# Kernel optimization log

Measured on AMD Instinct MI355X. Metric: run time of the kernel, lower is better.

Reference implementation:

```python
import jax, jax.numpy as jnp
import numpy as np

V, D, H, HS, BLK, L = 50257, 768, 12, 64, 1024, 6
B, S = 4, 1024
EPS = 1e-5


def layer_norm(x, g, b):
    mu = jnp.mean(x, axis=-1, keepdims=True)
    var = jnp.mean(jnp.square(x - mu), axis=-1, keepdims=True)
    return (x - mu) * jax.lax.rsqrt(var + EPS) * g + b


def setup_inputs() -> dict:
    key = jax.random.key(0)
    ks = jax.random.split(key, 24)
    s = 0.02
    inp = {
        "idx": jax.random.randint(ks[0], (B, S), 0, V),
        "tok_emb": jax.random.normal(ks[1], (V, D), jnp.float32) * s,
        "pos_emb": jax.random.normal(ks[2], (BLK, D), jnp.float32) * s,
        "Wq": jax.random.normal(ks[3], (L, H, D, HS), jnp.float32) * s,
        "bq": jnp.zeros((L, H, HS), jnp.float32),
        "Wk": jax.random.normal(ks[4], (L, H, D, HS), jnp.float32) * s,
        "bk": jnp.zeros((L, H, HS), jnp.float32),
        "Wv": jax.random.normal(ks[5], (L, H, D, HS), jnp.float32) * s,
        "bv": jnp.zeros((L, H, HS), jnp.float32),
        "Wproj": jax.random.normal(ks[6], (L, D, D), jnp.float32) * s,
        "bproj": jnp.zeros((L, D), jnp.float32),
        "ln1_g": jnp.ones((L, D), jnp.float32),
        "ln1_b": jnp.zeros((L, D), jnp.float32),
        "ln2_g": jnp.ones((L, D), jnp.float32),
        "ln2_b": jnp.zeros((L, D), jnp.float32),
        "Wf1": jax.random.normal(ks[7], (L, D, 4 * D), jnp.float32) * s,
        "bf1": jnp.zeros((L, 4 * D), jnp.float32),
        "Wf2": jax.random.normal(ks[8], (L, 4 * D, D), jnp.float32) * s,
        "bf2": jnp.zeros((L, D), jnp.float32),
        "lnf_g": jnp.ones((D,), jnp.float32),
        "lnf_b": jnp.zeros((D,), jnp.float32),
        "Wlm": jax.random.normal(ks[9], (V, D), jnp.float32) * s,
    }
    return inp


def attention(x, Wq, bq, Wk, bk, Wv, bv, Wproj, bproj):
    # x: [B,S,D]; per-head projections stacked over H
    q = jnp.einsum("bsd,hdk->bhsk", x, Wq) + bq[:, None, :]
    k = jnp.einsum("bsd,hdk->bhsk", x, Wk) + bk[:, None, :]
    v = jnp.einsum("bsd,hdk->bhsk", x, Wv) + bv[:, None, :]
    scores = jnp.einsum("bhsk,bhtk->bhst", q, k)  # [B,H,S,S]
    s = x.shape[1]
    mask = jnp.tril(jnp.ones((s, s), bool))
    # original: masked_fill(-inf) THEN divide by sqrt(head_size) -- equivalent
    scores = jnp.where(mask, scores, -jnp.inf) / np.sqrt(HS)
    w = jax.nn.softmax(scores, axis=-1)
    out = jnp.einsum("bhst,bhtk->bhsk", w, v)
    out = out.transpose(0, 2, 1, 3).reshape(x.shape[0], s, H * HS)
    return out @ Wproj + bproj


def reference(idx, tok_emb, pos_emb, Wq, bq, Wk, bk, Wv, bv, Wproj, bproj,
              ln1_g, ln1_b, ln2_g, ln2_b, Wf1, bf1, Wf2, bf2, lnf_g, lnf_b, Wlm):
    s = idx.shape[1]
    x = tok_emb[idx] + pos_emb[:s]
    for i in range(L):
        h = layer_norm(x, ln1_g[i], ln1_b[i])
        x = x + attention(h, Wq[i], bq[i], Wk[i], bk[i], Wv[i], bv[i], Wproj[i], bproj[i])
        h = layer_norm(x, ln2_g[i], ln2_b[i])
        x = x + (jax.nn.gelu(h @ Wf1[i] + bf1[i], approximate=False) @ Wf2[i] + bf2[i])
    x = layer_norm(x, lnf_g, lnf_b)
    logits = x @ Wlm.T  # [B,S,V]
    return logits
```

## Files before the change

### kernel.cpp

```cpp
#include <hip/hip_runtime.h>
#include <hip/hip_bf16.h>
#include <math.h>

#define D_MODEL 768
#define N_HEAD  12
#define HEAD    64
#define SEQ     1024
#define NLAYER  6
#define BATCH   4
#define NROWS   (BATCH*SEQ)
#define VOCAB   50257
#define VPAD    50432
#define DFFN    3072
#define DQKV    2304

typedef __attribute__((ext_vector_type(8))) __bf16 bf16x8;
typedef __attribute__((ext_vector_type(4))) float f32x4;
typedef __attribute__((ext_vector_type(4))) unsigned short u16x4;
typedef __attribute__((ext_vector_type(8))) unsigned short u16x8;

__device__ inline unsigned short f2bf(float x) {
    __hip_bfloat16 h = __float2bfloat16(x);
    return *reinterpret_cast<unsigned short*>(&h);
}

__global__ __launch_bounds__(256)
void embed_kernel(const int* __restrict__ idx, const float* __restrict__ tok,
                  const float* __restrict__ pos, float* __restrict__ x) {
    int row = blockIdx.x;
    int t = idx[row];
    int s = row & (SEQ - 1);
    const float* tp = tok + (size_t)t * D_MODEL;
    const float* pp = pos + (size_t)s * D_MODEL;
    float* xp = x + (size_t)row * D_MODEL;
    for (int i = threadIdx.x; i < D_MODEL; i += 256) xp[i] = tp[i] + pp[i];
}

__global__ __launch_bounds__(256)
void ln_kernel(const float* __restrict__ in, const float* __restrict__ gw,
               const float* __restrict__ bw, unsigned short* __restrict__ out) {
    int row = blockIdx.x;
    int tid = threadIdx.x;
    const float* x = in + (size_t)row * D_MODEL;
    float v0 = x[tid], v1 = x[tid + 256], v2 = x[tid + 512];
    float s  = v0 + v1 + v2;
    float sq = v0*v0 + v1*v1 + v2*v2;
    #pragma unroll
    for (int o = 1; o < 64; o <<= 1) { s += __shfl_xor(s, o); sq += __shfl_xor(sq, o); }
    __shared__ float red[8];
    int wave = tid >> 6;
    if ((tid & 63) == 0) { red[wave] = s; red[4 + wave] = sq; }
    __syncthreads();
    s  = red[0] + red[1] + red[2] + red[3];
    sq = red[4] + red[5] + red[6] + red[7];
    float mean = s * (1.0f / D_MODEL);
    float var  = sq * (1.0f / D_MODEL) - mean * mean;
    float rstd = rsqrtf(var + 1e-5f);
    unsigned short* op = out + (size_t)row * D_MODEL;
    op[tid]       = f2bf((v0 - mean) * rstd * gw[tid]       + bw[tid]);
    op[tid + 256] = f2bf((v1 - mean) * rstd * gw[tid + 256] + bw[tid + 256]);
    op[tid + 512] = f2bf((v2 - mean) * rstd * gw[tid + 512] + bw[tid + 512]);
}

template<int MODE>
__global__ __launch_bounds__(256)
void conv_transpose(const float* __restrict__ in, unsigned short* __restrict__ out,
                    int K, int N, size_t inLstride, size_t outLstride) {
    __shared__ float t[64][65];
    const int tid = threadIdx.x;
    const int n0 = blockIdx.x * 64, k0 = blockIdx.y * 64;
    const float* ip = in + blockIdx.z * inLstride;
    unsigned short* op = out + blockIdx.z * outLstride;
    {
        const int kk = tid >> 4, nq = tid & 15;
        #pragma unroll
        for (int p = 0; p < 4; ++p) {
            int k = kk + p * 16;
            float4 v;
            if (MODE == 0) v = *reinterpret_cast<const float4*>(&ip[(size_t)(k0 + k) * N + n0 + nq * 4]);
            else           v = *reinterpret_cast<const float4*>(&ip[((size_t)(n0 >> 6) * K + (k0 + k)) * 64 + nq * 4]);
            t[k][nq * 4 + 0] = v.x; t[k][nq * 4 + 1] = v.y;
            t[k][nq * 4 + 2] = v.z; t[k][nq * 4 + 3] = v.w;
        }
    }
    __syncthreads();
    {
        const int n = tid >> 2, kq = tid & 3;
        unsigned short buf[16];
        #pragma unroll
        for (int j = 0; j < 16; ++j) buf[j] = f2bf(t[kq * 16 + j][n]);
        unsigned short* dst = &op[(size_t)(n0 + n) * K + k0 + kq * 16];
        *reinterpret_cast<u16x8*>(dst)     = *reinterpret_cast<u16x8*>(&buf[0]);
        *reinterpret_cast<u16x8*>(dst + 8) = *reinterpret_cast<u16x8*>(&buf[8]);
    }
}

__global__ __launch_bounds__(256)
void conv_lm(const float* __restrict__ in, unsigned short* __restrict__ out) {
    const int nchunks = VPAD * D_MODEL / 4;
    const int vchunks = VOCAB * D_MODEL / 4;
    for (int i = blockIdx.x * 256 + threadIdx.x; i < nchunks; i += gridDim.x * 256) {
        u16x4 o;
        if (i < vchunks) {
            float4 v = reinterpret_cast<const float4*>(in)[i];
            o[0] = f2bf(v.x); o[1] = f2bf(v.y); o[2] = f2bf(v.z); o[3] = f2bf(v.w);
        } else { o[0] = 0; o[1] = 0; o[2] = 0; o[3] = 0; }
        reinterpret_cast<u16x4*>(out)[i] = o;
    }
}

__global__ __launch_bounds__(256)
void conv_bias(const float* __restrict__ bq, const float* __restrict__ bk,
               const float* __restrict__ bv, float* __restrict__ out) {
    int i = blockIdx.x * 256 + threadIdx.x;
    if (i >= NLAYER * DQKV) return;
    int l = i / DQKV, n = i % DQKV;
    float v;
    if (n < 768)        v = bq[l * 768 + n];
    else if (n < 1536)  v = bk[l * 768 + n - 768];
    else                v = bv[l * 768 + n - 1536];
    out[i] = v;
}

__global__ __launch_bounds__(512)
void gemm256_mfma(const unsigned short* __restrict__ A, const unsigned short* __restrict__ B,
                  float* __restrict__ C, int M, int N, int K) {
    __shared__ unsigned short smem[2 * 2 * 16384];
    const int nwg = gridDim.x;
    const int t0 = (blockIdx.x & 7) * (nwg >> 3) + (blockIdx.x >> 3);
    const int MT = M >> 8;
    const int NBX = nwg / MT;
    const int srsize = NBX * 8;
    const int sr = t0 / srsize;
    const int rem = t0 - sr * srsize;
    const int bx = rem >> 3;
    const int by = sr * 8 + (rem & 7);
    const int bm = by * 256, bn = bx * 256;
    const int tid = threadIdx.x;
    const int l = tid & 63, w = tid >> 6;
    const int wm = w >> 2, wn = w & 3;
    const int lr = l & 15, lc = l >> 4;
    f32x4 acc[8][4] = {};

    auto stage = [&](int k0, int buf) {
        #pragma unroll
        for (int p = 0; p < 4; ++p) {
            int d16 = p * 512 + tid;
            int row = d16 >> 3, cph = d16 & 7;
            int clog = cph ^ (row & 7);
            const unsigned short* ga = A + (size_t)(bm + row) * K + k0 + clog * 8;
            __builtin_amdgcn_global_load_lds(
                (const __attribute__((address_space(1))) unsigned int*)ga,
                (__attribute__((address_space(3))) unsigned int*)(&smem[buf * 32768 + d16 * 8]), 16, 0, 0);
        }
        #pragma unroll
        for (int p = 0; p < 4; ++p) {
            int d16 = p * 512 + tid;
            int row = d16 >> 3, cph = d16 & 7;
            int clog = cph ^ (row & 7);
            const unsigned short* gb = B + (size_t)(bn + row) * K + k0 + clog * 8;
            __builtin_amdgcn_global_load_lds(
                (const __attribute__((address_space(1))) unsigned int*)gb,
                (__attribute__((address_space(3))) unsigned int*)(&smem[buf * 32768 + 16384 + d16 * 8]), 16, 0, 0);
        }
    };

    auto compute = [&](int buf) {
        const unsigned short* Ab = &smem[buf * 32768];
        const unsigned short* Bb = &smem[buf * 32768 + 16384];
        bf16x8 bfr[2][4];
        #pragma unroll
        for (int ks = 0; ks < 2; ++ks)
            #pragma unroll
            for (int j = 0; j < 4; ++j) {
                int col = wn * 64 + j * 16 + lr;
                bfr[ks][j] = *reinterpret_cast<const bf16x8*>(
                    &Bb[col * 64 + (((ks * 4 + lc) ^ (col & 7)) * 8)]);
            }
        #pragma unroll
        for (int qm = 0; qm < 2; ++qm) {
            bf16x8 af[2][4];
            #pragma unroll
            for (int ks = 0; ks < 2; ++ks)
                #pragma unroll
                for (int mi = 0; mi < 4; ++mi) {
                    int row = wm * 128 + qm * 64 + mi * 16 + lr;
                    af[ks][mi] = *reinterpret_cast<const bf16x8*>(
                        &Ab[row * 64 + (((ks * 4 + lc) ^ (row & 7)) * 8)]);
                }
            __builtin_amdgcn_s_setprio(1);
            #pragma unroll
            for (int ks = 0; ks < 2; ++ks)
                #pragma unroll
                for (int mi = 0; mi < 4; ++mi)
                    #pragma unroll
                    for (int j = 0; j < 4; ++j)
                        acc[qm * 4 + mi][j] = __builtin_amdgcn_mfma_f32_16x16x32_bf16(
                            bfr[ks][j], af[ks][mi], acc[qm * 4 + mi][j], 0, 0, 0);
            __builtin_amdgcn_s_setprio(0);
        }
    };

    const int NT = K >> 6;
    stage(0, 0);
    asm volatile("s_waitcnt vmcnt(0)" ::: "memory");
    __builtin_amdgcn_s_barrier();
    for (int t = 0; t < NT; ++t) {
        const int cur = t & 1;
        if (t + 1 < NT) stage((t + 1) << 6, cur ^ 1);
        compute(cur);
        if (t + 1 < NT) {
            asm volatile("s_waitcnt vmcnt(0)" ::: "memory");
            __builtin_amdgcn_s_barrier();
        }
    }

    #pragma unroll
    for (int i = 0; i < 8; ++i) {
        const int row = bm + wm * 128 + i * 16 + lr;
        #pragma unroll
        for (int j = 0; j < 4; ++j) {
            const int colb = bn + wn * 64 + j * 16 + lc * 4;
            if (colb + 3 < N) {
                *reinterpret_cast<f32x4*>(&C[(size_t)row * N + colb]) = acc[i][j];
            } else {
                #pragma unroll
                for (int r = 0; r < 4; ++r)
                    if (colb + r < N) C[(size_t)row * N + colb + r] = acc[i][j][r];
            }
        }
    }
}

template<int BN, int OUTF , bool GELU, bool RES>
__global__ __launch_bounds__(256)
void gemm_sched(const unsigned short* __restrict__ A, const unsigned short* __restrict__ B,
                const float* __restrict__ bias, const float* __restrict__ res,
                void* __restrict__ Cout, int M, int N, int K) {
    constexpr int ABUF = 64 * 64;
    constexpr int TBUF = (64 + BN) * 64;
    constexpr int NI = BN / 32;
    __shared__ unsigned short smem[2 * TBUF];
    const int nwg = gridDim.x;
    const int t0 = (blockIdx.x & 7) * (nwg >> 3) + (blockIdx.x >> 3);
    const int MT = M >> 6;
    const int NBX = nwg / MT;
    const int srsize = NBX * 8;
    const int sr = t0 / srsize;
    const int rem = t0 - sr * srsize;
    const int bx = rem >> 3;
    const int by = sr * 8 + (rem & 7);
    const int bm = by * 64, bn = bx * BN;
    const int tid = threadIdx.x;
    const int l = tid & 63, w = tid >> 6;
    const int wr = (w & 1) * 32;
    const int wc = (w >> 1) * (BN / 2);
    const int lr = l & 15, lc = l >> 4;
    f32x4 acc[2][NI] = {};

    auto stage = [&](int k0, int buf) {
        #pragma unroll
        for (int p = 0; p < 2; ++p) {
            int d16 = p * 256 + tid;
            int row = d16 >> 3, cph = d16 & 7;
            int clog = cph ^ (row & 7);
            const unsigned short* ga = A + (size_t)(bm + row) * K + k0 + clog * 8;
            __builtin_amdgcn_global_load_lds(
                (const __attribute__((address_space(1))) unsigned int*)ga,
                (__attribute__((address_space(3))) unsigned int*)(&smem[buf * TBUF + d16 * 8]), 16, 0, 0);
        }
        #pragma unroll
        for (int p = 0; p < BN / 32; ++p) {
            int d16 = p * 256 + tid;
            int row = d16 >> 3, cph = d16 & 7;
            int clog = cph ^ (row & 7);
            const unsigned short* gb = B + (size_t)(bn + row) * K + k0 + clog * 8;
            __builtin_amdgcn_global_load_lds(
                (const __attribute__((address_space(1))) unsigned int*)gb,
                (__attribute__((address_space(3))) unsigned int*)(&smem[buf * TBUF + ABUF + d16 * 8]), 16, 0, 0);
        }
    };

    auto compute = [&](int buf) {
        const unsigned short* Ab = &smem[buf * TBUF];
        const unsigned short* Bb = &smem[buf * TBUF + ABUF];
        #pragma unroll
        for (int ks = 0; ks < 2; ++ks) {
            bf16x8 af[2], bfr[NI];
            #pragma unroll
            for (int mi = 0; mi < 2; ++mi) {
                int row = wr + mi * 16 + lr;
                af[mi] = *reinterpret_cast<const bf16x8*>(
                    &Ab[row * 64 + (((ks * 4 + lc) ^ (row & 7)) * 8)]);
            }
            #pragma unroll
            for (int ni = 0; ni < NI; ++ni) {
                int col = wc + ni * 16 + lr;
                bfr[ni] = *reinterpret_cast<const bf16x8*>(
                    &Bb[col * 64 + (((ks * 4 + lc) ^ (col & 7)) * 8)]);
            }
            __builtin_amdgcn_s_setprio(1);
            #pragma unroll
            for (int mi = 0; mi < 2; ++mi)
                #pragma unroll
                for (int ni = 0; ni < NI; ++ni)
                    acc[mi][ni] = __builtin_amdgcn_mfma_f32_16x16x32_bf16(
                        bfr[ni], af[mi], acc[mi][ni], 0, 0, 0);
            __builtin_amdgcn_s_setprio(0);
        }
    };

    const int NT = K >> 6;
    stage(0, 0);
    asm volatile("s_waitcnt vmcnt(0)" ::: "memory");
    __builtin_amdgcn_s_barrier();
    for (int t = 0; t < NT; ++t) {
        const int cur = t & 1;
        if (t + 1 < NT) stage((t + 1) << 6, cur ^ 1);
        compute(cur);
        if (t + 1 < NT) {
            asm volatile("s_waitcnt vmcnt(0)" ::: "memory");
            __builtin_amdgcn_s_barrier();
        }
    }

    #pragma unroll
    for (int mi = 0; mi < 2; ++mi) {
        const int row = bm + wr + mi * 16 + lr;
        #pragma unroll
        for (int ni = 0; ni < NI; ++ni) {
            const int colb = bn + wc + ni * 16 + lc * 4;
            f32x4 v = acc[mi][ni];
            if (bias) v += *reinterpret_cast<const f32x4*>(&bias[colb]);
            if (GELU) {
                #pragma unroll
                for (int r = 0; r < 4; ++r)
                    v[r] = 0.5f * v[r] * (1.0f + erff(v[r] * 0.70710678118654752f));
            }
            if (RES) v += *reinterpret_cast<const f32x4*>(&res[(size_t)row * N + colb]);
            if (OUTF == 0) {
                *reinterpret_cast<f32x4*>(&((float*)Cout)[(size_t)row * N + colb]) = v;
            } else {
                u16x4 o;
                o[0] = f2bf(v[0]); o[1] = f2bf(v[1]); o[2] = f2bf(v[2]); o[3] = f2bf(v[3]);
                *reinterpret_cast<u16x4*>(&((unsigned short*)Cout)[(size_t)row * N + colb]) = o;
            }
        }
    }
}

__global__ __launch_bounds__(512)
void attn_mfma(const unsigned short* __restrict__ qkv, unsigned short* __restrict__ ao) {
    const int qt = gridDim.x - 1 - blockIdx.x;
    const int h = blockIdx.y, b = blockIdx.z;
    const int tid = threadIdx.x;
    const int w = tid >> 6, l = tid & 63;
    const int c = l & 15, g = l >> 4;

    __shared__ unsigned short Ks[2][32 * 64];
    __shared__ unsigned short Vt[2][64 * 40];
    __shared__ unsigned int   Ps[8][16 * 20];

    const unsigned short* base = qkv + (size_t)(b * SEQ) * DQKV + h * HEAD;
    const int q0 = qt * 128 + w * 16;

    bf16x8 qf[2];
    {
        const unsigned short* qp = base + (size_t)(q0 + c) * DQKV + g * 8;
        qf[0] = *reinterpret_cast<const bf16x8*>(qp);
        qf[1] = *reinterpret_cast<const bf16x8*>(qp + 32);
    }

    f32x4 o_acc[4] = {};
    float m_run[4]  = {-INFINITY, -INFINITY, -INFINITY, -INFINITY};
    float l_run[4]  = {0.f, 0.f, 0.f, 0.f};

    const int srow = tid >> 4, sch8 = tid & 15;
    const int scj = sch8 >> 1, sh = sch8 & 1;
    const int vd = tid & 63, vw = tid >> 6;

    u16x4 kreg;
    unsigned short vreg[4];
    auto loadKV = [&](int kt) {
        kreg = *reinterpret_cast<const u16x4*>(
            base + (size_t)(kt * 32 + srow) * DQKV + 768 + sch8 * 4);
        #pragma unroll
        for (int j = 0; j < 4; ++j)
            vreg[j] = base[(size_t)(kt * 32 + vw * 4 + j) * DQKV + 1536 + vd];
    };

    const int nkt = 4 * qt + 4;
    loadKV(0);
    for (int kt = 0; kt < nkt; ++kt) {
        const int bf = kt & 1;
        *reinterpret_cast<u16x4*>(&Ks[bf][srow * 64 + ((scj ^ (srow & 7)) * 8) + sh * 4]) = kreg;
        {
            uint2 pk;
            pk.x = vreg[0] | ((unsigned)vreg[1] << 16);
            pk.y = vreg[2] | ((unsigned)vreg[3] << 16);
            *reinterpret_cast<uint2*>(&Vt[bf][vd * 40 + vw * 4]) = pk;
        }
        __syncthreads();
        if (kt + 1 < nkt) loadKV(kt + 1);

        f32x4 s_acc[2] = {};
        #pragma unroll
        for (int t = 0; t < 2; ++t) {
            const int kr = t * 16 + c;
            #pragma unroll
            for (int ks = 0; ks < 2; ++ks) {
                bf16x8 kf = *reinterpret_cast<const bf16x8*>(
                    &Ks[bf][kr * 64 + (((ks * 4 + g) ^ (kr & 7)) * 8)]);
                s_acc[t] = __builtin_amdgcn_mfma_f32_16x16x32_bf16(qf[ks], kf, s_acc[t], 0, 0, 0);
            }
        }
        float sc[2][4];
        #pragma unroll
        for (int t = 0; t < 2; ++t) {
            const int kglob = kt * 32 + t * 16 + c;
            #pragma unroll
            for (int r = 0; r < 4; ++r) {
                float v = s_acc[t][r] * 0.125f;
                sc[t][r] = (kglob > q0 + g * 4 + r) ? -1e30f : v;
            }
        }
        float pout[2][4];
        #pragma unroll
        for (int r = 0; r < 4; ++r) {
            float tmax = fmaxf(sc[0][r], sc[1][r]);
            #pragma unroll
            for (int ms = 1; ms < 16; ms <<= 1) tmax = fmaxf(tmax, __shfl_xor(tmax, ms));
            float mnew = fmaxf(m_run[r], tmax);
            float alpha = __expf(m_run[r] - mnew);
            float p0 = __expf(sc[0][r] - mnew);
            float p1 = __expf(sc[1][r] - mnew);
            float psum = p0 + p1;
            #pragma unroll
            for (int ms = 1; ms < 16; ms <<= 1) psum += __shfl_xor(psum, ms);
            l_run[r] = l_run[r] * alpha + psum;
            m_run[r] = mnew;
            #pragma unroll
            for (int dt = 0; dt < 4; ++dt) o_acc[dt][r] *= alpha;
            pout[0][r] = p0; pout[1][r] = p1;
        }
        #pragma unroll
        for (int t = 0; t < 2; ++t) {
            #pragma unroll
            for (int r = 0; r < 4; ++r) {
                int my = f2bf(pout[t][r]);
                int part = __shfl_xor(my, 1);
                unsigned int word = (c & 1) ? ((unsigned)(part & 0xffff) | ((unsigned)my << 16))
                                            : ((unsigned)(my & 0xffff) | ((unsigned)part << 16));
                Ps[w][(g * 4 + r) * 20 + t * 8 + (c >> 1)] = word;
            }
        }
        uint4 praw = *reinterpret_cast<const uint4*>(&Ps[w][c * 20 + g * 4]);
        bf16x8 pf = *reinterpret_cast<const bf16x8*>(&praw);
        #pragma unroll
        for (int dt = 0; dt < 4; ++dt) {
            bf16x8 vf = *reinterpret_cast<const bf16x8*>(&Vt[bf][(dt * 16 + c) * 40 + g * 8]);
            o_acc[dt] = __builtin_amdgcn_mfma_f32_16x16x32_bf16(pf, vf, o_acc[dt], 0, 0, 0);
        }
    }

    float inv[4];
    #pragma unroll
    for (int r = 0; r < 4; ++r) inv[r] = 1.0f / l_run[r];
    #pragma unroll
    for (int r = 0; r < 4; ++r) {
        unsigned short* op = ao + (size_t)(b * SEQ + q0 + g * 4 + r) * D_MODEL + h * HEAD + c;
        #pragma unroll
        for (int dt = 0; dt < 4; ++dt)
            op[dt * 16] = f2bf(o_acc[dt][r] * inv[r]);
    }
}

extern "C" void kernel_launch(void* const* d_in, const int* in_sizes, int n_in,
                              void* d_out, int out_size, void* d_ws, size_t ws_size,
                              hipStream_t stream) {
    const int*   idx     = (const int*)  d_in[0];
    const float* tok_emb = (const float*)d_in[1];
    const float* pos_emb = (const float*)d_in[2];
    const float* Wq      = (const float*)d_in[3];
    const float* bq      = (const float*)d_in[4];
    const float* Wk      = (const float*)d_in[5];
    const float* bk      = (const float*)d_in[6];
    const float* Wv      = (const float*)d_in[7];
    const float* bv      = (const float*)d_in[8];
    const float* Wproj   = (const float*)d_in[9];
    const float* bproj   = (const float*)d_in[10];
    const float* ln1g    = (const float*)d_in[11];
    const float* ln1b    = (const float*)d_in[12];
    const float* ln2g    = (const float*)d_in[13];
    const float* ln2b    = (const float*)d_in[14];
    const float* Wf1     = (const float*)d_in[15];
    const float* bf1     = (const float*)d_in[16];
    const float* Wf2     = (const float*)d_in[17];
    const float* bf2     = (const float*)d_in[18];
    const float* lnfg    = (const float*)d_in[19];
    const float* lnfb    = (const float*)d_in[20];
    const float* Wlm     = (const float*)d_in[21];
    float* outp = (float*)d_out;

    char* basep = (char*)d_ws;
    size_t off = 0;
    auto alloc = [&](size_t bytes) -> void* {
        void* p = basep + off;
        off = (off + bytes + 255) & ~(size_t)255;
        return p;
    };
    float*          x      = (float*)         alloc((size_t)NROWS * D_MODEL * 4);
    unsigned short* qkv    = (unsigned short*)alloc((size_t)NROWS * DQKV * 2);
    unsigned short* hb     = (unsigned short*)alloc((size_t)NROWS * D_MODEL * 2);
    unsigned short* ao     = (unsigned short*)alloc((size_t)NROWS * D_MODEL * 2);
    unsigned short* mid    = (unsigned short*)alloc((size_t)NROWS * DFFN * 2);
    unsigned short* Wqkvb  = (unsigned short*)alloc((size_t)NLAYER * DQKV * D_MODEL * 2);
    unsigned short* Wprojb = (unsigned short*)alloc((size_t)NLAYER * D_MODEL * D_MODEL * 2);
    unsigned short* Wf1b   = (unsigned short*)alloc((size_t)NLAYER * DFFN * D_MODEL * 2);
    unsigned short* Wf2b   = (unsigned short*)alloc((size_t)NLAYER * D_MODEL * DFFN * 2);
    unsigned short* Wlmb   = (unsigned short*)alloc((size_t)VPAD * D_MODEL * 2);
    float*          bqkv   = (float*)         alloc((size_t)NLAYER * DQKV * 4);

    dim3 blk(256);

    conv_lm<<<2048, blk, 0, stream>>>(Wlm, Wlmb);
    conv_transpose<1><<<dim3(12, 12, 6), blk, 0, stream>>>(Wq, Wqkvb,             768, 768,  (size_t)768*768,  (size_t)DQKV*768);
    conv_transpose<1><<<dim3(12, 12, 6), blk, 0, stream>>>(Wk, Wqkvb + 768*768,   768, 768,  (size_t)768*768,  (size_t)DQKV*768);
    conv_transpose<1><<<dim3(12, 12, 6), blk, 0, stream>>>(Wv, Wqkvb + 2*768*768, 768, 768,  (size_t)768*768,  (size_t)DQKV*768);
    conv_transpose<0><<<dim3(12, 12, 6), blk, 0, stream>>>(Wproj, Wprojb,         768, 768,  (size_t)768*768,  (size_t)768*768);
    conv_transpose<0><<<dim3(48, 12, 6), blk, 0, stream>>>(Wf1, Wf1b,             768, 3072, (size_t)768*3072, (size_t)3072*768);
    conv_transpose<0><<<dim3(12, 48, 6), blk, 0, stream>>>(Wf2, Wf2b,             3072, 768, (size_t)3072*768, (size_t)768*3072);
    conv_bias<<<(NLAYER * DQKV + 255) / 256, blk, 0, stream>>>(bq, bk, bv, bqkv);

    embed_kernel<<<NROWS, blk, 0, stream>>>(idx, tok_emb, pos_emb, x);

    dim3 gqkv(64 * 18);
    dim3 g768s(64 * 12);
    dim3 g3072(64 * 24);
    dim3 ga(SEQ / 128, N_HEAD, BATCH);

    for (int li = 0; li < NLAYER; ++li) {
        ln_kernel<<<NROWS, blk, 0, stream>>>(x, ln1g + li * D_MODEL, ln1b + li * D_MODEL, hb);

        gemm_sched<128, 1, false, false><<<gqkv, blk, 0, stream>>>(
            hb, Wqkvb + (size_t)li * DQKV * D_MODEL, bqkv + li * DQKV, nullptr,
            qkv, NROWS, DQKV, D_MODEL);

        attn_mfma<<<ga, dim3(512), 0, stream>>>(qkv, ao);

        gemm_sched<64, 0, false, true><<<g768s, blk, 0, stream>>>(
            ao, Wprojb + (size_t)li * D_MODEL * D_MODEL, bproj + li * D_MODEL, x,
            x, NROWS, D_MODEL, D_MODEL);

        ln_kernel<<<NROWS, blk, 0, stream>>>(x, ln2g + li * D_MODEL, ln2b + li * D_MODEL, hb);

        gemm_sched<128, 1, true, false><<<g3072, blk, 0, stream>>>(
            hb, Wf1b + (size_t)li * DFFN * D_MODEL, bf1 + li * DFFN, nullptr,
            mid, NROWS, DFFN, D_MODEL);

        gemm_sched<64, 0, false, true><<<g768s, blk, 0, stream>>>(
            mid, Wf2b + (size_t)li * D_MODEL * DFFN, bf2 + li * D_MODEL, x,
            x, NROWS, D_MODEL, DFFN);
    }

    ln_kernel<<<NROWS, blk, 0, stream>>>(x, lnfg, lnfb, hb);

    dim3 gl((VPAD / 256) * (NROWS / 256));
    gemm256_mfma<<<gl, dim3(512), 0, stream>>>(hb, Wlmb, outp, NROWS, VOCAB, D_MODEL);
}
```

Baseline: 1.922 ms.

## Fuse embedding with first layernorm and single-buffer LM-head GEMM

Merges the embedding add with layer 0's first layernorm, which removes one launch and one full re-read of x. The 256x256 LM-head GEMM drops from double-buffered to single-buffered LDS, halving its shared memory, likely to allow more resident workgroups, at the cost of no longer overlapping loads with MFMA compute. Its logits are now written with nontemporal stores to avoid polluting the cache with the large output. These are several unrelated changes bundled together.

After: 2.337 ms. +21.6%, slower.

```diff
diff --git a/kernel.cpp b/kernel.cpp
--- a/kernel.cpp
+++ b/kernel.cpp
@@ -25,15 +25,38 @@
 }
 
 __global__ __launch_bounds__(256)
-void embed_kernel(const int* __restrict__ idx, const float* __restrict__ tok,
-                  const float* __restrict__ pos, float* __restrict__ x) {
+void embed_ln_kernel(const int* __restrict__ idx, const float* __restrict__ tok,
+                     const float* __restrict__ pos, const float* __restrict__ gw,
+                     const float* __restrict__ bw, float* __restrict__ x,
+                     unsigned short* __restrict__ hb) {
     int row = blockIdx.x;
     int t = idx[row];
     int s = row & (SEQ - 1);
+    int tid = threadIdx.x;
     const float* tp = tok + (size_t)t * D_MODEL;
     const float* pp = pos + (size_t)s * D_MODEL;
+    float v0 = tp[tid]       + pp[tid];
+    float v1 = tp[tid + 256] + pp[tid + 256];
+    float v2 = tp[tid + 512] + pp[tid + 512];
     float* xp = x + (size_t)row * D_MODEL;
-    for (int i = threadIdx.x; i < D_MODEL; i += 256) xp[i] = tp[i] + pp[i];
+    xp[tid] = v0; xp[tid + 256] = v1; xp[tid + 512] = v2;
+    float sm  = v0 + v1 + v2;
+    float sq = v0*v0 + v1*v1 + v2*v2;
+    #pragma unroll
+    for (int o = 1; o < 64; o <<= 1) { sm += __shfl_xor(sm, o); sq += __shfl_xor(sq, o); }
+    __shared__ float red[8];
+    int wave = tid >> 6;
+    if ((tid & 63) == 0) { red[wave] = sm; red[4 + wave] = sq; }
+    __syncthreads();
+    sm = red[0] + red[1] + red[2] + red[3];
+    sq = red[4] + red[5] + red[6] + red[7];
+    float mean = sm * (1.0f / D_MODEL);
+    float var  = sq * (1.0f / D_MODEL) - mean * mean;
+    float rstd = rsqrtf(var + 1e-5f);
+    unsigned short* op = hb + (size_t)row * D_MODEL;
+    op[tid]       = f2bf((v0 - mean) * rstd * gw[tid]       + bw[tid]);
+    op[tid + 256] = f2bf((v1 - mean) * rstd * gw[tid + 256] + bw[tid + 256]);
+    op[tid + 512] = f2bf((v2 - mean) * rstd * gw[tid + 512] + bw[tid + 512]);
 }
 
 __global__ __launch_bounds__(256)
@@ -125,7 +148,7 @@
 __global__ __launch_bounds__(512)
 void gemm256_mfma(const unsigned short* __restrict__ A, const unsigned short* __restrict__ B,
                   float* __restrict__ C, int M, int N, int K) {
-    __shared__ unsigned short smem[2 * 2 * 16384];
+    __shared__ unsigned short smem[2 * 16384];
     const int nwg = gridDim.x;
     const int t0 = (blockIdx.x & 7) * (nwg >> 3) + (blockIdx.x >> 3);
     const int MT = M >> 8;
@@ -142,7 +165,7 @@
     const int lr = l & 15, lc = l >> 4;
     f32x4 acc[8][4] = {};
 
-    auto stage = [&](int k0, int buf) {
+    auto stage = [&](int k0) {
         #pragma unroll
         for (int p = 0; p < 4; ++p) {
             int d16 = p * 512 + tid;
@@ -151,7 +174,7 @@
             const unsigned short* ga = A + (size_t)(bm + row) * K + k0 + clog * 8;
             __builtin_amdgcn_global_load_lds(
                 (const __attribute__((address_space(1))) unsigned int*)ga,
-                (__attribute__((address_space(3))) unsigned int*)(&smem[buf * 32768 + d16 * 8]), 16, 0, 0);
+                (__attribute__((address_space(3))) unsigned int*)(&smem[d16 * 8]), 16, 0, 0);
         }
         #pragma unroll
         for (int p = 0; p < 4; ++p) {
@@ -161,13 +184,13 @@
             const unsigned short* gb = B + (size_t)(bn + row) * K + k0 + clog * 8;
             __builtin_amdgcn_global_load_lds(
                 (const __attribute__((address_space(1))) unsigned int*)gb,
-                (__attribute__((address_space(3))) unsigned int*)(&smem[buf * 32768 + 16384 + d16 * 8]), 16, 0, 0);
+                (__attribute__((address_space(3))) unsigned int*)(&smem[16384 + d16 * 8]), 16, 0, 0);
         }
     };
 
-    auto compute = [&](int buf) {
-        const unsigned short* Ab = &smem[buf * 32768];
-        const unsigned short* Bb = &smem[buf * 32768 + 16384];
+    auto compute = [&]() {
+        const unsigned short* Ab = &smem[0];
+        const unsigned short* Bb = &smem[16384];
         bf16x8 bfr[2][4];
         #pragma unroll
         for (int ks = 0; ks < 2; ++ks)
@@ -202,17 +225,12 @@
     };
 
     const int NT = K >> 6;
-    stage(0, 0);
-    asm volatile("s_waitcnt vmcnt(0)" ::: "memory");
-    __builtin_amdgcn_s_barrier();
     for (int t = 0; t < NT; ++t) {
-        const int cur = t & 1;
-        if (t + 1 < NT) stage((t + 1) << 6, cur ^ 1);
-        compute(cur);
-        if (t + 1 < NT) {
-            asm volatile("s_waitcnt vmcnt(0)" ::: "memory");
-            __builtin_amdgcn_s_barrier();
-        }
+        stage(t << 6);
+        asm volatile("s_waitcnt vmcnt(0)" ::: "memory");
+        __builtin_amdgcn_s_barrier();
+        compute();
+        if (t + 1 < NT) __builtin_amdgcn_s_barrier();
     }
 
     #pragma unroll
@@ -222,7 +240,8 @@
         for (int j = 0; j < 4; ++j) {
             const int colb = bn + wn * 64 + j * 16 + lc * 4;
             if (colb + 3 < N) {
-                *reinterpret_cast<f32x4*>(&C[(size_t)row * N + colb]) = acc[i][j];
+                __builtin_nontemporal_store(acc[i][j],
+                    reinterpret_cast<f32x4*>(&C[(size_t)row * N + colb]));
             } else {
                 #pragma unroll
                 for (int r = 0; r < 4; ++r)
@@ -532,7 +551,7 @@
     conv_transpose<0><<<dim3(12, 48, 6), blk, 0, stream>>>(Wf2, Wf2b,             3072, 768, (size_t)3072*768, (size_t)768*3072);
     conv_bias<<<(NLAYER * DQKV + 255) / 256, blk, 0, stream>>>(bq, bk, bv, bqkv);
 
-    embed_kernel<<<NROWS, blk, 0, stream>>>(idx, tok_emb, pos_emb, x);
+    embed_ln_kernel<<<NROWS, blk, 0, stream>>>(idx, tok_emb, pos_emb, ln1g, ln1b, x, hb);
 
     dim3 gqkv(64 * 18);
     dim3 g768s(64 * 12);
@@ -540,7 +559,8 @@
     dim3 ga(SEQ / 128, N_HEAD, BATCH);
 
     for (int li = 0; li < NLAYER; ++li) {
-        ln_kernel<<<NROWS, blk, 0, stream>>>(x, ln1g + li * D_MODEL, ln1b + li * D_MODEL, hb);
+        if (li > 0)
+            ln_kernel<<<NROWS, blk, 0, stream>>>(x, ln1g + li * D_MODEL, ln1b + li * D_MODEL, hb);
 
         gemm_sched<128, 1, false, false><<<gqkv, blk, 0, stream>>>(
             hb, Wqkvb + (size_t)li * DQKV * D_MODEL, bqkv + li * DQKV, nullptr,
```
